# Kernel optimization log

Measured on AMD Instinct MI355X. Metric: run time of the kernel, lower is better.

The kernel has to match this reference:

```python
import jax, jax.numpy as jnp
import numpy as np

EPS = 1e-5

def layer_norm(x, g, b):
    mu = jnp.mean(x, axis=-1, keepdims=True)
    var = jnp.mean(jnp.square(x - mu), axis=-1, keepdims=True)
    return (x - mu) * jax.lax.rsqrt(var + EPS) * g + b

def setup_inputs() -> dict:
    key = jax.random.key(0)
    ks = jax.random.split(key, 16)
    B, S, D, H, T = 8, 1024, 512, 8, 6
    Dff = 4 * D
    s = 0.02
    return {
        "x": jax.random.normal(ks[0], (B, S, D), jnp.float32),
        "signal_type_ids": jax.random.randint(ks[1], (B, S), 0, T, jnp.int32),
        "emb": jax.random.normal(ks[2], (T, D), jnp.float32) * s,
        "in_proj_w": jax.random.normal(ks[3], (3 * D, D), jnp.float32) * s,
        "in_proj_b": jnp.zeros((3 * D,), jnp.float32),
        "out_proj_w": jax.random.normal(ks[4], (D, D), jnp.float32) * s,
        "out_proj_b": jnp.zeros((D,), jnp.float32),
        "ln1_g": jnp.ones((D,), jnp.float32),
        "ln1_b": jnp.zeros((D,), jnp.float32),
        "ln2_g": jnp.ones((D,), jnp.float32),
        "ln2_b": jnp.zeros((D,), jnp.float32),
        "w1": jax.random.normal(ks[5], (Dff, D), jnp.float32) * s,
        "b1": jnp.zeros((Dff,), jnp.float32),
        "w2": jax.random.normal(ks[6], (D, Dff), jnp.float32) * s,
        "b2": jnp.zeros((D,), jnp.float32),
    }

def reference(x, signal_type_ids, emb, in_proj_w, in_proj_b, out_proj_w, out_proj_b,
              ln1_g, ln1_b, ln2_g, ln2_b, w1, b1, w2, b2):
    B, S, D = x.shape
    H = 8
    hd = D // H
    # embedding add
    x = x + emb[signal_type_ids]
    # pre-norm MHA (need_weights=True path, average_attn_weights=True)
    xn = layer_norm(x, ln1_g, ln1_b)
    qkv = xn @ in_proj_w.T + in_proj_b            # [B,S,3D]
    q, k, v = jnp.split(qkv, 3, axis=-1)
    q = q.reshape(B, S, H, hd)
    k = k.reshape(B, S, H, hd)
    v = v.reshape(B, S, H, hd)
    scores = jnp.einsum("bqhd,bkhd->bhqk", q, k) / jnp.sqrt(jnp.asarray(hd, x.dtype))
    attn = jax.nn.softmax(scores, axis=-1)        # [B,H,S,S]
    attn_weights = jnp.mean(attn, axis=1)         # averaged over heads [B,S,S]
    ctx = jnp.einsum("bhqk,bkhd->bqhd", attn, v).reshape(B, S, D)
    attn_out = ctx @ out_proj_w.T + out_proj_b
    x = x + attn_out
    # FFN with exact GELU (torch nn.GELU default)
    h = layer_norm(x, ln2_g, ln2_b)
    h = jax.nn.gelu(h @ w1.T + b1, approximate=False)
    x = x + h @ w2.T + b2
    return x, attn_weights
```

## Files before the change

### kernel.cpp

```cpp
#include <hip/hip_runtime.h>
#include <math.h>

constexpr int CB = 8;
constexpr int CS = 1024;
constexpr int CD = 512;
constexpr int CH = 8;
constexpr int CHD = 64;
constexpr int CDFF = 2048;
constexpr int NROW = CB * CS;

typedef unsigned short u16;
typedef unsigned int u32;
typedef __attribute__((ext_vector_type(8))) short short8;
typedef __attribute__((ext_vector_type(8))) unsigned short ushort8v;
typedef __attribute__((ext_vector_type(4))) float floatx4;

__device__ inline u16 f2bf(float f) {
    union { float f; unsigned u; } v; v.f = f;
    unsigned u = v.u + 0x7FFFu + ((v.u >> 16) & 1u);
    return (u16)(u >> 16);
}
__device__ inline float bf2f(u16 h) {
    union { unsigned u; float f; } v; v.u = ((unsigned)h) << 16;
    return v.f;
}

__device__ inline void gload16(const u16* g, u16* l) {
    __builtin_amdgcn_global_load_lds(
        (const __attribute__((address_space(1))) u32*)g,
        (__attribute__((address_space(3))) u32*)l, 16, 0, 0);
}

__global__ __launch_bounds__(256) void ln_kernel(
    const float* __restrict__ x, const int* __restrict__ ids,
    const float* __restrict__ emb,
    const float* __restrict__ g, const float* __restrict__ beta,
    float* __restrict__ xr_out, u16* __restrict__ xn_out)
{
    __shared__ float red1[4], red2[4];
    __shared__ float mu_s, ri_s;
    int row = blockIdx.x;
    int tid = threadIdx.x;
    int d0 = tid * 2;
    const float* xrow = x + (size_t)row * CD;
    float2 xv = *(const float2*)(xrow + d0);
    float v0 = xv.x, v1 = xv.y;
    if (emb) {
        int id = ids[row];
        float2 ev = *(const float2*)(emb + (size_t)id * CD + d0);
        v0 += ev.x; v1 += ev.y;
    }
    float s1 = v0 + v1;
    float s2 = v0 * v0 + v1 * v1;
    for (int off = 32; off > 0; off >>= 1) {
        s1 += __shfl_down(s1, off, 64);
        s2 += __shfl_down(s2, off, 64);
    }
    int wave = tid >> 6;
    if ((tid & 63) == 0) { red1[wave] = s1; red2[wave] = s2; }
    __syncthreads();
    if (tid == 0) {
        float t1 = red1[0] + red1[1] + red1[2] + red1[3];
        float t2 = red2[0] + red2[1] + red2[2] + red2[3];
        float mu = t1 / CD;
        float var = t2 / CD - mu * mu;
        mu_s = mu;
        ri_s = rsqrtf(var + 1e-5f);
    }
    __syncthreads();
    float mu = mu_s, ri = ri_s;
    if (xr_out) {
        float2 o; o.x = v0; o.y = v1;
        *(float2*)(xr_out + (size_t)row * CD + d0) = o;
    }
    float2 gv = *(const float2*)(g + d0);
    float2 bv = *(const float2*)(beta + d0);
    float n0 = (v0 - mu) * ri * gv.x + bv.x;
    float n1 = (v1 - mu) * ri * gv.y + bv.y;
    u32 pk = (u32)f2bf(n0) | ((u32)f2bf(n1) << 16);
    *(u32*)(xn_out + (size_t)row * CD + d0) = pk;
}

__global__ __launch_bounds__(256) void conv4_kernel(
    const float* __restrict__ s0, const float* __restrict__ s1,
    const float* __restrict__ s2, const float* __restrict__ s3,
    u16* __restrict__ dst)
{
    size_t i = ((size_t)blockIdx.x * 256 + threadIdx.x) * 8;
    const float* src;
    size_t off;
    if (i < 786432)        { src = s0; off = i; }
    else if (i < 1048576)  { src = s1; off = i - 786432; }
    else if (i < 2097152)  { src = s2; off = i - 1048576; }
    else                   { src = s3; off = i - 2097152; }
    float4 a = *(const float4*)(src + off);
    float4 b = *(const float4*)(src + off + 4);
    ushort8v o;
    o[0] = f2bf(a.x); o[1] = f2bf(a.y); o[2] = f2bf(a.z); o[3] = f2bf(a.w);
    o[4] = f2bf(b.x); o[5] = f2bf(b.y); o[6] = f2bf(b.z); o[7] = f2bf(b.w);
    *(ushort8v*)(dst + i) = o;
}

template <int ACT, int RES, int OUTBF>
__global__ __launch_bounds__(256) void gemm_mfma(
    const u16* __restrict__ A, const u16* __restrict__ W,
    const float* __restrict__ bias, const float* __restrict__ res,
    void* __restrict__ Cout, int M, int N, int K)
{
    __shared__ u16 As[128 * 32];
    __shared__ u16 Bs[128 * 32];
    int t = threadIdx.x;
    int lane = t & 63;
    int w = t >> 6;
    int m0 = blockIdx.x * 128;
    int n0 = blockIdx.y * 128;
    int col = lane & 15;
    int quad = lane >> 4;
    int wm = w & 1, wn = w >> 1;

    const u16* ag = A + (size_t)(m0 + (t >> 2)) * K + (t & 3) * 8;
    const u16* ag2 = ag + (size_t)64 * K;
    const u16* bg = W + (size_t)(n0 + (t >> 2)) * K + (t & 3) * 8;
    const u16* bg2 = bg + (size_t)64 * K;
    u16* la = As + w * 512;
    u16* lb = Bs + w * 512;

    floatx4 acc[4][4];
#pragma unroll
    for (int i = 0; i < 4; i++)
#pragma unroll
        for (int j = 0; j < 4; j++) acc[i][j] = (floatx4){0.f, 0.f, 0.f, 0.f};

    for (int kt = 0; kt < K; kt += 32) {
        gload16(ag + kt, la);
        gload16(ag2 + kt, la + 2048);
        gload16(bg + kt, lb);
        gload16(bg2 + kt, lb + 2048);
        __syncthreads();
        short8 af[4], bf[4];
#pragma unroll
        for (int mi = 0; mi < 4; mi++)
            af[mi] = *(const short8*)&As[(wm * 64 + mi * 16 + col) * 32 + quad * 8];
#pragma unroll
        for (int ni = 0; ni < 4; ni++)
            bf[ni] = *(const short8*)&Bs[(wn * 64 + ni * 16 + col) * 32 + quad * 8];
#pragma unroll
        for (int mi = 0; mi < 4; mi++)
#pragma unroll
            for (int ni = 0; ni < 4; ni++)
                acc[mi][ni] = __builtin_amdgcn_mfma_f32_16x16x32_bf16(
                    af[mi], bf[ni], acc[mi][ni], 0, 0, 0);
        __syncthreads();
    }

#pragma unroll
    for (int mi = 0; mi < 4; mi++)
#pragma unroll
        for (int ni = 0; ni < 4; ni++) {
            int c = n0 + wn * 64 + ni * 16 + col;
            float bv = bias[c];
#pragma unroll
            for (int r = 0; r < 4; r++) {
                int m = m0 + wm * 64 + mi * 16 + quad * 4 + r;
                float v = acc[mi][ni][r] + bv;
                if (ACT == 1) v = 0.5f * v * (1.0f + erff(v * 0.70710678118654752f));
                if (RES) v += res[(size_t)m * N + c];
                if (OUTBF) ((u16*)Cout)[(size_t)m * N + c] = f2bf(v);
                else       ((float*)Cout)[(size_t)m * N + c] = v;
            }
        }
}

template <int ACT, int RES, int OUTBF>
__global__ __launch_bounds__(256) void gemm_mfma64(
    const u16* __restrict__ A, const u16* __restrict__ W,
    const float* __restrict__ bias, const float* __restrict__ res,
    void* __restrict__ Cout, int M, int N, int K)
{
    __shared__ u16 As[64 * 32];
    __shared__ u16 Bs[128 * 32];
    int t = threadIdx.x;
    int lane = t & 63;
    int w = t >> 6;
    int m0 = blockIdx.x * 64;
    int n0 = blockIdx.y * 128;
    int col = lane & 15;
    int quad = lane >> 4;

    const u16* ag = A + (size_t)(m0 + (t >> 2)) * K + (t & 3) * 8;
    const u16* bg = W + (size_t)(n0 + (t >> 2)) * K + (t & 3) * 8;
    const u16* bg2 = bg + (size_t)64 * K;
    u16* la = As + w * 512;
    u16* lb = Bs + w * 512;

    floatx4 acc[4][2];
#pragma unroll
    for (int i = 0; i < 4; i++)
#pragma unroll
        for (int j = 0; j < 2; j++) acc[i][j] = (floatx4){0.f, 0.f, 0.f, 0.f};

    for (int kt = 0; kt < K; kt += 32) {
        gload16(ag + kt, la);
        gload16(bg + kt, lb);
        gload16(bg2 + kt, lb + 2048);
        __syncthreads();
        short8 af[4], bf[2];
#pragma unroll
        for (int mi = 0; mi < 4; mi++)
            af[mi] = *(const short8*)&As[(mi * 16 + col) * 32 + quad * 8];
#pragma unroll
        for (int ni = 0; ni < 2; ni++)
            bf[ni] = *(const short8*)&Bs[(w * 32 + ni * 16 + col) * 32 + quad * 8];
#pragma unroll
        for (int mi = 0; mi < 4; mi++)
#pragma unroll
            for (int ni = 0; ni < 2; ni++)
                acc[mi][ni] = __builtin_amdgcn_mfma_f32_16x16x32_bf16(
                    af[mi], bf[ni], acc[mi][ni], 0, 0, 0);
        __syncthreads();
    }

#pragma unroll
    for (int mi = 0; mi < 4; mi++)
#pragma unroll
        for (int ni = 0; ni < 2; ni++) {
            int c = n0 + w * 32 + ni * 16 + col;
            float bv = bias[c];
#pragma unroll
            for (int r = 0; r < 4; r++) {
                int m = m0 + mi * 16 + quad * 4 + r;
                float v = acc[mi][ni][r] + bv;
                if (ACT == 1) v = 0.5f * v * (1.0f + erff(v * 0.70710678118654752f));
                if (RES) v += res[(size_t)m * N + c];
                if (OUTBF) ((u16*)Cout)[(size_t)m * N + c] = f2bf(v);
                else       ((float*)Cout)[(size_t)m * N + c] = v;
            }
        }
}

__global__ __launch_bounds__(256) void vt_kernel(
    const u16* __restrict__ qkvb, u16* __restrict__ vt)
{
    __shared__ u16 tile[64][72];
    int b = blockIdx.x >> 4;
    int s0 = (blockIdx.x & 15) * 64;
    int h = blockIdx.y;
    int t = threadIdx.x;
    int r = t >> 2;
    int c0 = (t & 3) * 16;
    const u16* src = qkvb + (size_t)(b * CS + s0 + r) * 1536 + 2 * CD + h * CHD + c0;
    *(ushort8v*)&tile[r][c0] = *(const ushort8v*)src;
    *(ushort8v*)&tile[r][c0 + 8] = *(const ushort8v*)(src + 8);
    __syncthreads();
    u16* dst = vt + (((size_t)b * CH + h) * CHD + r) * CS + s0 + c0;
    ushort8v lo, hi;
#pragma unroll
    for (int j = 0; j < 8; j++) { lo[j] = tile[c0 + j][r]; hi[j] = tile[c0 + 8 + j][r]; }
    *(ushort8v*)dst = lo;
    *(ushort8v*)(dst + 8) = hi;
}

__global__ __launch_bounds__(256, 2) void attn_fused_kernel(
    const u16* __restrict__ qkvb, const u16* __restrict__ vt,
    u16* __restrict__ Se, float* __restrict__ Lout,
    u16* __restrict__ ctx, int b0)
{
    __shared__ u16 Qs[2][64 * 32];
    __shared__ u16 Ks[2][2][64 * 32];
    __shared__ u16 Vs[2][2][64 * 32];
    __shared__ u16 S[64][72];
    __shared__ float rs[4][4][16];

    int t = threadIdx.x;
    int lane = t & 63;
    int w = t >> 6;
    int col = lane & 15;
    int quad = lane >> 4;
    int bid = blockIdx.x;
    int xcd = bid & 7;
    int j = bid >> 3;
    int bhl = xcd * 4 + (j >> 4);
    int qt = j & 15;
    int lb = bhl >> 3, h = bhl & 7;
    int b = b0 + lb;
    int q0 = qt * 64;
    int bh = b * CH + h;
    size_t splane = (size_t)(lb * CH + h) * CS * CS;

    int srow = t >> 2;
    int scol = (t & 3) * 8;

    const u16* ksrc0 = qkvb + (size_t)(b * CS + srow) * 1536 + CD + h * CHD + scol;
    const u16* vsrc0 = vt + ((size_t)bh * CHD + srow) * CS + scol;

    {
        const u16* qsrc = qkvb + (size_t)(b * CS + q0 + srow) * 1536 + h * CHD + scol;
        gload16(qsrc, Qs[0] + w * 512);
        gload16(qsrc + 32, Qs[1] + w * 512);
        gload16(ksrc0, Ks[0][0] + w * 512);
        gload16(ksrc0 + 32, Ks[0][1] + w * 512);
        gload16(vsrc0, Vs[0][0] + w * 512);
        gload16(vsrc0 + 32, Vs[0][1] + w * 512);
    }
    __syncthreads();

    short8 qf[2][4];
#pragma unroll
    for (int dsl = 0; dsl < 2; dsl++)
#pragma unroll
        for (int nq = 0; nq < 4; nq++)
            qf[dsl][nq] = *(const short8*)&Qs[dsl][(nq * 16 + col) * 32 + quad * 8];

    floatx4 acc[4];
#pragma unroll
    for (int i = 0; i < 4; i++) acc[i] = (floatx4){0.f, 0.f, 0.f, 0.f};
    float esum[4] = {0.f, 0.f, 0.f, 0.f};

    for (int kc = 0; kc < 16; kc++) {
        int cur = kc & 1;
        short8 kf0 = *(const short8*)&Ks[cur][0][(w * 16 + col) * 32 + quad * 8];
        short8 kf1 = *(const short8*)&Ks[cur][1][(w * 16 + col) * 32 + quad * 8];
#pragma unroll
        for (int nq = 0; nq < 4; nq++) {
            floatx4 c = {0.f, 0.f, 0.f, 0.f};
            c = __builtin_amdgcn_mfma_f32_16x16x32_bf16(kf0, qf[0][nq], c, 0, 0, 0);
            c = __builtin_amdgcn_mfma_f32_16x16x32_bf16(kf1, qf[1][nq], c, 0, 0, 0);
            float e0 = __expf(c[0] * 0.125f);
            float e1 = __expf(c[1] * 0.125f);
            float e2 = __expf(c[2] * 0.125f);
            float e3 = __expf(c[3] * 0.125f);
            esum[nq] += (e0 + e1) + (e2 + e3);
            union { float f; u32 u; } a0, a1, a2, a3;
            a0.f = e0; a1.f = e1; a2.f = e2; a3.f = e3;
            u32 p0 = (a0.u >> 16) | (a1.u & 0xFFFF0000u);
            u32 p1 = (a2.u >> 16) | (a3.u & 0xFFFF0000u);
            u32* sp = (u32*)&S[nq * 16 + col][w * 16 + quad * 4];
            sp[0] = p0; sp[1] = p1;
            u32* gp = (u32*)(Se + splane + (size_t)(q0 + nq * 16 + col) * CS
                             + kc * 64 + w * 16 + quad * 4);
            gp[0] = p0; gp[1] = p1;
        }
        __syncthreads();

        if (kc < 15) {
            int ko = (kc + 1) * 64;
            const u16* ks = ksrc0 + (size_t)ko * 1536;
            gload16(ks, Ks[cur ^ 1][0] + w * 512);
            gload16(ks + 32, Ks[cur ^ 1][1] + w * 512);
            gload16(vsrc0 + ko, Vs[cur ^ 1][0] + w * 512);
            gload16(vsrc0 + ko + 32, Vs[cur ^ 1][1] + w * 512);
        }

        short8 sf0 = *(const short8*)&S[w * 16 + col][quad * 8];
        short8 sf1 = *(const short8*)&S[w * 16 + col][32 + quad * 8];
#pragma unroll
        for (int nd = 0; nd < 4; nd++) {
            short8 vf0 = *(const short8*)&Vs[cur][0][(nd * 16 + col) * 32 + quad * 8];
            short8 vf1 = *(const short8*)&Vs[cur][1][(nd * 16 + col) * 32 + quad * 8];
            acc[nd] = __builtin_amdgcn_mfma_f32_16x16x32_bf16(sf0, vf0, acc[nd], 0, 0, 0);
            acc[nd] = __builtin_amdgcn_mfma_f32_16x16x32_bf16(sf1, vf1, acc[nd], 0, 0, 0);
        }
        __syncthreads();
    }

#pragma unroll
    for (int nq = 0; nq < 4; nq++) {
        float v = esum[nq];
        v += __shfl_xor(v, 16, 64);
        v += __shfl_xor(v, 32, 64);
        if (quad == 0) rs[w][nq][col] = v;
    }
    __syncthreads();
    if (t < 64) {
        int nq = t >> 4, c2 = t & 15;
        float L = rs[0][nq][c2] + rs[1][nq][c2] + rs[2][nq][c2] + rs[3][nq][c2];
        Lout[((size_t)bh << 10) + q0 + nq * 16 + c2] = L;
    }

    float li[4];
#pragma unroll
    for (int r = 0; r < 4; r++) {
        int cr = quad * 4 + r;
        li[r] = 1.0f / (rs[0][w][cr] + rs[1][w][cr] + rs[2][w][cr] + rs[3][w][cr]);
    }
    u16* cb = ctx + ((size_t)(b * CS) + q0 + w * 16 + quad * 4) * CD + h * CHD + col;
#pragma unroll
    for (int nd = 0; nd < 4; nd++)
#pragma unroll
        for (int r = 0; r < 4; r++)
            cb[(size_t)r * CD + nd * 16] = f2bf(acc[nd][r] * li[r]);
}

__global__ __launch_bounds__(256, 8) void attn_aw_kernel(
    const u16* __restrict__ Se, const float* __restrict__ Lin,
    float* __restrict__ aw_out, int b0)
{
    int bq = blockIdx.x;
    int bl = bq >> 9;
    int b = b0 + bl;
    int q = (bq & 511) * 2 + (threadIdx.x >> 7);
    int k0 = (threadIdx.x & 127) * 8;

    float acc[8];
#pragma unroll
    for (int i = 0; i < 8; i++) acc[i] = 0.f;

#pragma unroll
    for (int h = 0; h < CH; h++) {
        float linv = 0.125f / Lin[(((size_t)(b * CH + h)) << 10) + q];
        const u16* sp = Se + ((size_t)(bl * CH + h) * CS + q) * CS + k0;
        ushort8v e = *(const ushort8v*)sp;
#pragma unroll
        for (int i = 0; i < 8; i++) acc[i] += bf2f(e[i]) * linv;
    }
    float* ap = aw_out + ((size_t)(b * CS) + q) * CS + k0;
    *(float4*)ap = make_float4(acc[0], acc[1], acc[2], acc[3]);
    *(float4*)(ap + 4) = make_float4(acc[4], acc[5], acc[6], acc[7]);
}

extern "C" void kernel_launch(void* const* d_in, const int* in_sizes, int n_in,
                              void* d_out, int out_size, void* d_ws, size_t ws_size,
                              hipStream_t stream)
{
    const float* x    = (const float*)d_in[0];
    const int*   ids  = (const int*)d_in[1];
    const float* emb  = (const float*)d_in[2];
    const float* inw  = (const float*)d_in[3];
    const float* inb  = (const float*)d_in[4];
    const float* ow   = (const float*)d_in[5];
    const float* ob   = (const float*)d_in[6];
    const float* g1   = (const float*)d_in[7];
    const float* be1  = (const float*)d_in[8];
    const float* g2   = (const float*)d_in[9];
    const float* be2  = (const float*)d_in[10];
    const float* w1   = (const float*)d_in[11];
    const float* b1   = (const float*)d_in[12];
    const float* w2   = (const float*)d_in[13];
    const float* b2   = (const float*)d_in[14];

    float* out_x  = (float*)d_out;
    float* out_aw = out_x + (size_t)CB * CS * CD;

    char* p = (char*)d_ws;
    float* xr   = (float*)p; p += (size_t)NROW * CD * 4;
    float* x2   = (float*)p; p += (size_t)NROW * CD * 4;
    u16* xnb    = (u16*)p;   p += (size_t)NROW * CD * 2;
    u16* qkvb   = (u16*)p;   p += (size_t)NROW * 3 * CD * 2;
    u16* ctxb   = (u16*)p;   p += (size_t)NROW * CD * 2;
    u16* hidb   = (u16*)p;   p += (size_t)NROW * CDFF * 2;
    u16* inwb   = (u16*)p;   p += (size_t)3 * CD * CD * 2;
    u16* owb    = (u16*)p;   p += (size_t)CD * CD * 2;
    u16* w1b    = (u16*)p;   p += (size_t)CDFF * CD * 2;
    u16* w2b    = (u16*)p;   p += (size_t)CD * CDFF * 2;
    float* Lbuf = (float*)p; p += (size_t)CB * CH * CS * 4;
    u16* Se     = (u16*)p;   p += (size_t)(CB / 2) * CH * CS * CS * 2;

    u16* vtb = hidb;

    dim3 blk(256);
    conv4_kernel<<<(3 * CD * CD + CD * CD + 2 * CDFF * CD) / 2048, blk, 0, stream>>>(
        inw, ow, w1, w2, inwb);
    ln_kernel<<<NROW, blk, 0, stream>>>(x, ids, emb, g1, be1, xr, xnb);
    gemm_mfma<0, 0, 1><<<dim3(NROW / 128, (3 * CD) / 128), blk, 0, stream>>>(
        xnb, inwb, inb, nullptr, qkvb, NROW, 3 * CD, CD);
    vt_kernel<<<dim3(CB * (CS / 64), CH), blk, 0, stream>>>(qkvb, vtb);
    for (int half = 0; half < 2; half++) {
        int b0 = half * 4;
        attn_fused_kernel<<<512, blk, 0, stream>>>(qkvb, vtb, Se, Lbuf, ctxb, b0);
        attn_aw_kernel<<<2048, blk, 0, stream>>>(Se, Lbuf, out_aw, b0);
    }
    gemm_mfma64<0, 1, 0><<<dim3(NROW / 64, CD / 128), blk, 0, stream>>>(
        ctxb, owb, ob, xr, x2, NROW, CD, CD);
    ln_kernel<<<NROW, blk, 0, stream>>>(x2, nullptr, nullptr, g2, be2, nullptr, xnb);
    gemm_mfma<1, 0, 1><<<dim3(NROW / 128, CDFF / 128), blk, 0, stream>>>(
        xnb, w1b, b1, nullptr, hidb, NROW, CDFF, CD);
    gemm_mfma64<0, 1, 0><<<dim3(NROW / 64, CD / 128), blk, 0, stream>>>(
        hidb, w2b, b2, x2, out_x, NROW, CD, CDFF);
}
```

Before: 325.1 us.

## Double-buffer GEMM LDS tiles and use tanh-form GELU approximation

Both MFMA GEMM kernels now keep two LDS buffers and issue the next K tile's global-to-LDS loads before computing on the current tile. This removes one barrier per iteration and lets loads overlap with MFMA work, at the cost of twice the LDS per block. The exact erf GELU in the epilogue is replaced by the tanh approximation written as a sigmoid with a fast exp, which is cheaper but deviates slightly from the exact GELU.

```diff
diff --git a/kernel.cpp b/kernel.cpp
--- a/kernel.cpp
+++ b/kernel.cpp
@@ -23,6 +23,12 @@
 __device__ inline float bf2f(u16 h) {
     union { unsigned u; float f; } v; v.u = ((unsigned)h) << 16;
     return v.f;
+}
+
+__device__ inline float gelu_fast(float v) {
+    float u = v * (1.0f + 0.044715f * v * v);
+    float e = __expf(-1.5957691216057308f * u);
+    return v / (1.0f + e);
 }
 
 __device__ inline void gload16(const u16* g, u16* l) {
@@ -107,8 +113,8 @@
     const float* __restrict__ bias, const float* __restrict__ res,
     void* __restrict__ Cout, int M, int N, int K)
 {
-    __shared__ u16 As[128 * 32];
-    __shared__ u16 Bs[128 * 32];
+    __shared__ u16 As[2][128 * 32];
+    __shared__ u16 Bs[2][128 * 32];
     int t = threadIdx.x;
     int lane = t & 63;
     int w = t >> 6;
@@ -117,13 +123,18 @@
     int col = lane & 15;
     int quad = lane >> 4;
     int wm = w & 1, wn = w >> 1;
+    int lo = w * 512;
 
     const u16* ag = A + (size_t)(m0 + (t >> 2)) * K + (t & 3) * 8;
     const u16* ag2 = ag + (size_t)64 * K;
     const u16* bg = W + (size_t)(n0 + (t >> 2)) * K + (t & 3) * 8;
     const u16* bg2 = bg + (size_t)64 * K;
-    u16* la = As + w * 512;
-    u16* lb = Bs + w * 512;
+
+    gload16(ag, As[0] + lo);
+    gload16(ag2, As[0] + 2048 + lo);
+    gload16(bg, Bs[0] + lo);
+    gload16(bg2, Bs[0] + 2048 + lo);
+    __syncthreads();
 
     floatx4 acc[4][4];
 #pragma unroll
@@ -131,19 +142,23 @@
 #pragma unroll
         for (int j = 0; j < 4; j++) acc[i][j] = (floatx4){0.f, 0.f, 0.f, 0.f};
 
-    for (int kt = 0; kt < K; kt += 32) {
-        gload16(ag + kt, la);
-        gload16(ag2 + kt, la + 2048);
-        gload16(bg + kt, lb);
-        gload16(bg2 + kt, lb + 2048);
-        __syncthreads();
+    int nk = K >> 5;
+    for (int kt = 0; kt < nk; kt++) {
+        int cur = kt & 1;
+        if (kt + 1 < nk) {
+            int ko = (kt + 1) * 32;
+            gload16(ag + ko, As[cur ^ 1] + lo);
+            gload16(ag2 + ko, As[cur ^ 1] + 2048 + lo);
+            gload16(bg + ko, Bs[cur ^ 1] + lo);
+            gload16(bg2 + ko, Bs[cur ^ 1] + 2048 + lo);
+        }
         short8 af[4], bf[4];
 #pragma unroll
         for (int mi = 0; mi < 4; mi++)
-            af[mi] = *(const short8*)&As[(wm * 64 + mi * 16 + col) * 32 + quad * 8];
+            af[mi] = *(const short8*)&As[cur][(wm * 64 + mi * 16 + col) * 32 + quad * 8];
 #pragma unroll
         for (int ni = 0; ni < 4; ni++)
-            bf[ni] = *(const short8*)&Bs[(wn * 64 + ni * 16 + col) * 32 + quad * 8];
+            bf[ni] = *(const short8*)&Bs[cur][(wn * 64 + ni * 16 + col) * 32 + quad * 8];
 #pragma unroll
         for (int mi = 0; mi < 4; mi++)
 #pragma unroll
@@ -163,7 +178,7 @@
             for (int r = 0; r < 4; r++) {
                 int m = m0 + wm * 64 + mi * 16 + quad * 4 + r;
                 float v = acc[mi][ni][r] + bv;
-                if (ACT == 1) v = 0.5f * v * (1.0f + erff(v * 0.70710678118654752f));
+                if (ACT == 1) v = gelu_fast(v);
                 if (RES) v += res[(size_t)m * N + c];
                 if (OUTBF) ((u16*)Cout)[(size_t)m * N + c] = f2bf(v);
                 else       ((float*)Cout)[(size_t)m * N + c] = v;
@@ -177,8 +192,8 @@
     const float* __restrict__ bias, const float* __restrict__ res,
     void* __restrict__ Cout, int M, int N, int K)
 {
-    __shared__ u16 As[64 * 32];
-    __shared__ u16 Bs[128 * 32];
+    __shared__ u16 As[2][64 * 32];
+    __shared__ u16 Bs[2][128 * 32];
     int t = threadIdx.x;
     int lane = t & 63;
     int w = t >> 6;
@@ -186,12 +201,16 @@
     int n0 = blockIdx.y * 128;
     int col = lane & 15;
     int quad = lane >> 4;
+    int lo = w * 512;
 
     const u16* ag = A + (size_t)(m0 + (t >> 2)) * K + (t & 3) * 8;
     const u16* bg = W + (size_t)(n0 + (t >> 2)) * K + (t & 3) * 8;
     const u16* bg2 = bg + (size_t)64 * K;
-    u16* la = As + w * 512;
-    u16* lb = Bs + w * 512;
+
+    gload16(ag, As[0] + lo);
+    gload16(bg, Bs[0] + lo);
+    gload16(bg2, Bs[0] + 2048 + lo);
+    __syncthreads();
 
     floatx4 acc[4][2];
 #pragma unroll
@@ -199,18 +218,22 @@
 #pragma unroll
         for (int j = 0; j < 2; j++) acc[i][j] = (floatx4){0.f, 0.f, 0.f, 0.f};
 
-    for (int kt = 0; kt < K; kt += 32) {
-        gload16(ag + kt, la);
-        gload16(bg + kt, lb);
-        gload16(bg2 + kt, lb + 2048);
-        __syncthreads();
+    int nk = K >> 5;
+    for (int kt = 0; kt < nk; kt++) {
+        int cur = kt & 1;
+        if (kt + 1 < nk) {
+            int ko = (kt + 1) * 32;
+            gload16(ag + ko, As[cur ^ 1] + lo);
+            gload16(bg + ko, Bs[cur ^ 1] + lo);
+            gload16(bg2 + ko, Bs[cur ^ 1] + 2048 + lo);
+        }
         short8 af[4], bf[2];
 #pragma unroll
         for (int mi = 0; mi < 4; mi++)
-            af[mi] = *(const short8*)&As[(mi * 16 + col) * 32 + quad * 8];
+            af[mi] = *(const short8*)&As[cur][(mi * 16 + col) * 32 + quad * 8];
 #pragma unroll
         for (int ni = 0; ni < 2; ni++)
-            bf[ni] = *(const short8*)&Bs[(w * 32 + ni * 16 + col) * 32 + quad * 8];
+            bf[ni] = *(const short8*)&Bs[cur][(w * 32 + ni * 16 + col) * 32 + quad * 8];
 #pragma unroll
         for (int mi = 0; mi < 4; mi++)
 #pragma unroll
@@ -230,7 +253,7 @@
             for (int r = 0; r < 4; r++) {
                 int m = m0 + mi * 16 + quad * 4 + r;
                 float v = acc[mi][ni][r] + bv;
-                if (ACT == 1) v = 0.5f * v * (1.0f + erff(v * 0.70710678118654752f));
+                if (ACT == 1) v = gelu_fast(v);
                 if (RES) v += res[(size_t)m * N + c];
                 if (OUTBF) ((u16*)Cout)[(size_t)m * N + c] = f2bf(v);
                 else       ((float*)Cout)[(size_t)m * N + c] = v;
```

New measurement: 315.2 us. 1.03x faster.
